# Kernel tuning notes

Hardware: AMD Instinct MI355X
Metric: run time of the kernel (lower is better)

## Reference

```python
import jax, jax.numpy as jnp
import numpy as np
from jax import lax


def setup_inputs() -> dict:
    key = jax.random.key(0)
    ks = jax.random.split(key, 8)
    B, N, q = 16, 4096, 256
    sc = float(1.0 / np.sqrt(q))
    return {
        "u": jax.random.normal(ks[0], (B, N, q), jnp.float32),
        "a": jax.random.normal(ks[1], (q,), jnp.float32),  # diag of A
        "W_B": jax.random.normal(ks[2], (q, q), jnp.float32) * sc,
        "b_B": jax.random.normal(ks[3], (q,), jnp.float32) * sc,
        "W_C": jax.random.normal(ks[4], (q, q), jnp.float32) * sc,
        "b_C": jax.random.normal(ks[5], (q,), jnp.float32) * sc,
        "W_D": jax.random.normal(ks[6], (q, q), jnp.float32) * sc,
        "b_D": jax.random.normal(ks[7], (q,), jnp.float32) * sc,
    }


def _solve_im(u, a, W_B, b_B, dt):
    """IM solver. A is diagonal, so M_inv is four diagonal blocks:
    new_x = s*x - dt*s*a*z ; new_z = dt*s*x + s*z, with s = 1/(1+dt^2*a).
    Forcing F = M_inv @ [dt*B(u); 0] -> (dt*s*Bu, dt^2*s*Bu)."""
    s = 1.0 / (1.0 + dt * dt * a)  # (q,)
    Bu = jnp.einsum("bnq,pq->bnp", u, W_B) + b_B  # (B,N,q), torch Linear: u @ W^T + b
    f_x = (dt * s) * Bu
    f_z = (dt * dt * s) * Bu
    dsa = dt * s * a
    ds = dt * s

    def step(carry, f):
        x, z = carry
        fx, fz = f
        x_new = s * x - dsa * z + fx
        z_new = ds * x + s * z + fz
        return (x_new, z_new), z_new

    Bsz, _, q = u.shape
    init = (jnp.zeros((Bsz, q), u.dtype), jnp.zeros((Bsz, q), u.dtype))
    # scan over time axis
    _, z_t = lax.scan(step, init, (jnp.moveaxis(f_x, 1, 0), jnp.moveaxis(f_z, 1, 0)))
    return jnp.moveaxis(z_t, 0, 1)  # (B,N,q) -- the out[..., size:] half


def reference(u, a, W_B, b_B, W_C, b_C, W_D, b_D):
    N = u.shape[1]
    dt = 1.0 / N
    y = _solve_im(u, a, W_B, b_B, dt)
    x = (jnp.einsum("bnq,pq->bnp", y, W_C) + b_C) + (jnp.einsum("bnq,pq->bnp", u, W_D) + b_D)
    x = jax.nn.gelu(x, approximate=False)  # torch GELU default = exact erf
    # GLU(concat([x, x], -1)) == x * sigmoid(x)
    out = x * jax.nn.sigmoid(x) + u
    return (out, y)
```

## Files before the change

kernel.cpp:

```cpp
#include <hip/hip_runtime.h>
#include <hip/hip_bf16.h>
#include <cstdint>

typedef __bf16 bf16_t;
typedef __bf16 bf16x8 __attribute__((ext_vector_type(8)));
typedef float f32x4 __attribute__((ext_vector_type(4)));

#define B_SZ 16
#define N_SZ 4096
#define Q_SZ 256
#define M_TOT (B_SZ * N_SZ)
#define DT (1.0f / 4096.0f)
#define LDST 40
#define CHUNKS 16
#define CLEN (N_SZ / CHUNKS)

__device__ __forceinline__ bf16x8 load8f(const float* p) {
  const float4 v0 = *(const float4*)p;
  const float4 v1 = *(const float4*)(p + 4);
  bf16x8 v;
  v[0] = (bf16_t)v0.x; v[1] = (bf16_t)v0.y; v[2] = (bf16_t)v0.z; v[3] = (bf16_t)v0.w;
  v[4] = (bf16_t)v1.x; v[5] = (bf16_t)v1.y; v[6] = (bf16_t)v1.z; v[7] = (bf16_t)v1.w;
  return v;
}

__device__ __forceinline__ void kloop(const float* __restrict__ Ap,
                                      const float* __restrict__ Bp,
                                      int m0, int n0, int t,
                                      bf16_t* As, bf16_t* Bs, f32x4 acc[4][4]) {
  const int r = t >> 2, cc = t & 3;
  const int lane = t & 63, ln = lane & 15, quad = lane >> 4;
  const int wave = t >> 6;
  const int wm = (wave & 1) * 64, wn = (wave >> 1) * 64;

  for (int k0 = 0; k0 < Q_SZ; k0 += 32) {
#pragma unroll
    for (int i = 0; i < 2; ++i) {
      const int row = r + i * 64;
      const int col = k0 + cc * 8;
      *(bf16x8*)(As + row * LDST + cc * 8) =
          load8f(Ap + (size_t)(m0 + row) * Q_SZ + col);
      *(bf16x8*)(Bs + row * LDST + cc * 8) =
          load8f(Bp + (size_t)(n0 + row) * Q_SZ + col);
    }
    __syncthreads();
    bf16x8 af[4], bv[4];
#pragma unroll
    for (int mi = 0; mi < 4; ++mi) {
      af[mi] = *(const bf16x8*)(As + (wm + mi * 16 + ln) * LDST + quad * 8);
      bv[mi] = *(const bf16x8*)(Bs + (wn + mi * 16 + ln) * LDST + quad * 8);
    }
#pragma unroll
    for (int mi = 0; mi < 4; ++mi)
#pragma unroll
      for (int ni = 0; ni < 4; ++ni)
        acc[mi][ni] = __builtin_amdgcn_mfma_f32_16x16x32_bf16(af[mi], bv[ni],
                                                              acc[mi][ni], 0, 0, 0);
    __syncthreads();
  }
}

__global__ __launch_bounds__(256) void gemm1_kernel(
    const float* __restrict__ u, const float* __restrict__ WB,
    const float* __restrict__ a, const float* __restrict__ bB,
    float* __restrict__ fx) {
  __shared__ __align__(16) bf16_t As[128 * LDST];
  __shared__ __align__(16) bf16_t Bs[128 * LDST];
  const int t = threadIdx.x;
  const int m0 = blockIdx.x * 128, n0 = blockIdx.y * 128;
  f32x4 acc[4][4] = {};
  kloop(u, WB, m0, n0, t, As, Bs, acc);

  const int lane = t & 63, ln = lane & 15, quad = lane >> 4;
  const int wave = t >> 6;
  const int wm = (wave & 1) * 64, wn = (wave >> 1) * 64;
#pragma unroll
  for (int ni = 0; ni < 4; ++ni) {
    const int gp = n0 + wn + ni * 16 + ln;
    const float av = a[gp];
    const float s = 1.0f / (1.0f + DT * DT * av);
    const float sc = DT * s;
    const float bb = bB[gp];
#pragma unroll
    for (int mi = 0; mi < 4; ++mi) {
      const int gm = m0 + wm + mi * 16 + quad * 4;
#pragma unroll
      for (int r2 = 0; r2 < 4; ++r2)
        fx[(size_t)(gm + r2) * Q_SZ + gp] = sc * (acc[mi][ni][r2] + bb);
    }
  }
}

#define PF 8

__global__ __launch_bounds__(256) void scan1_kernel(
    const float* __restrict__ fx, const float* __restrict__ a,
    float* __restrict__ ex, float* __restrict__ ez) {
  const int g = blockIdx.x * 256 + threadIdx.x;
  const int p = g & 255, c = (g >> 8) & (CHUNKS - 1), b = g >> 12;
  const float av = a[p];
  const float s = 1.0f / (1.0f + DT * DT * av);
  const float dsa = DT * s * av, dss = DT * s;
  float x = 0.f, z = 0.f;
  const float* fp = fx + ((size_t)b * N_SZ + c * CLEN) * Q_SZ + p;
  float buf[PF], nbuf[PF];
#pragma unroll
  for (int j = 0; j < PF; ++j) buf[j] = fp[(size_t)j * Q_SZ];
  for (int n = 0; n < CLEN; n += PF) {
    if (n + PF < CLEN) {
#pragma unroll
      for (int j = 0; j < PF; ++j) nbuf[j] = fp[(size_t)(n + PF + j) * Q_SZ];
    }
#pragma unroll
    for (int j = 0; j < PF; ++j) {
      const float f = buf[j];
      const float xn = fmaf(s, x, fmaf(-dsa, z, f));
      const float zn = fmaf(dss, x, fmaf(s, z, DT * f));
      x = xn; z = zn;
    }
#pragma unroll
    for (int j = 0; j < PF; ++j) buf[j] = nbuf[j];
  }
  ex[g] = x; ez[g] = z;
}

__global__ __launch_bounds__(256) void scan2_kernel(
    const float* __restrict__ a, const float* __restrict__ ex,
    const float* __restrict__ ez, float* __restrict__ ix, float* __restrict__ iz) {
  const int g = blockIdx.x * 256 + threadIdx.x;
  const int p = g & 255, b = g >> 8;
  const float av = a[p];
  const float s = 1.0f / (1.0f + DT * DT * av);
  float m00 = s, m01 = -DT * s * av, m10 = DT * s, m11 = s;
#pragma unroll
  for (int i = 0; i < 8; ++i) {
    const float a00 = fmaf(m00, m00, m01 * m10);
    const float a01 = m01 * (m00 + m11);
    const float a10 = m10 * (m00 + m11);
    const float a11 = fmaf(m11, m11, m01 * m10);
    m00 = a00; m01 = a01; m10 = a10; m11 = a11;
  }
  float x = 0.f, z = 0.f;
  for (int c = 0; c < CHUNKS; ++c) {
    const size_t idx = ((size_t)b * CHUNKS + c) * Q_SZ + p;
    ix[idx] = x; iz[idx] = z;
    const float xn = fmaf(m00, x, fmaf(m01, z, ex[idx]));
    const float zn = fmaf(m10, x, fmaf(m11, z, ez[idx]));
    x = xn; z = zn;
  }
}

__global__ __launch_bounds__(256) void scan3_kernel(
    const float* __restrict__ a, const float* __restrict__ ix,
    const float* __restrict__ iz, float* __restrict__ yf) {
  const int g = blockIdx.x * 256 + threadIdx.x;
  const int p = g & 255, c = (g >> 8) & (CHUNKS - 1), b = g >> 12;
  const float av = a[p];
  const float s = 1.0f / (1.0f + DT * DT * av);
  const float dsa = DT * s * av, dss = DT * s;
  float x = ix[g], z = iz[g];
  float* yp = yf + ((size_t)b * N_SZ + c * CLEN) * Q_SZ + p;
  float buf[PF], nbuf[PF];
#pragma unroll
  for (int j = 0; j < PF; ++j) buf[j] = yp[(size_t)j * Q_SZ];
  for (int n = 0; n < CLEN; n += PF) {
    if (n + PF < CLEN) {
#pragma unroll
      for (int j = 0; j < PF; ++j) nbuf[j] = yp[(size_t)(n + PF + j) * Q_SZ];
    }
#pragma unroll
    for (int j = 0; j < PF; ++j) {
      const float f = buf[j];
      const float xn = fmaf(s, x, fmaf(-dsa, z, f));
      const float zn = fmaf(dss, x, fmaf(s, z, DT * f));
      x = xn; z = zn;
      yp[(size_t)(n + j) * Q_SZ] = zn;
    }
#pragma unroll
    for (int j = 0; j < PF; ++j) buf[j] = nbuf[j];
  }
}

__global__ __launch_bounds__(256) void scan_mono_kernel(
    const float* __restrict__ a, float* __restrict__ yf) {
  const int g = blockIdx.x * 256 + threadIdx.x;
  const int p = g & 255, b = g >> 8;
  const float av = a[p];
  const float s = 1.0f / (1.0f + DT * DT * av);
  const float dsa = DT * s * av, dss = DT * s;
  float x = 0.f, z = 0.f;
  float* yp = yf + (size_t)b * N_SZ * Q_SZ + p;
  float buf[PF], nbuf[PF];
#pragma unroll
  for (int j = 0; j < PF; ++j) buf[j] = yp[(size_t)j * Q_SZ];
  for (int n = 0; n < N_SZ; n += PF) {
    if (n + PF < N_SZ) {
#pragma unroll
      for (int j = 0; j < PF; ++j) nbuf[j] = yp[(size_t)(n + PF + j) * Q_SZ];
    }
#pragma unroll
    for (int j = 0; j < PF; ++j) {
      const float f = buf[j];
      const float xn = fmaf(s, x, fmaf(-dsa, z, f));
      const float zn = fmaf(dss, x, fmaf(s, z, DT * f));
      x = xn; z = zn;
      yp[(size_t)(n + j) * Q_SZ] = zn;
    }
#pragma unroll
    for (int j = 0; j < PF; ++j) buf[j] = nbuf[j];
  }
}

__global__ __launch_bounds__(256) void gemm2_kernel(
    const float* __restrict__ y, const float* __restrict__ WC,
    const float* __restrict__ u, const float* __restrict__ WD,
    const float* __restrict__ bC, const float* __restrict__ bD,
    float* __restrict__ out0) {
  __shared__ __align__(16) bf16_t As[128 * LDST];
  __shared__ __align__(16) bf16_t Bs[128 * LDST];
  const int t = threadIdx.x;
  const int m0 = blockIdx.x * 128, n0 = blockIdx.y * 128;
  f32x4 acc[4][4] = {};
  kloop(y, WC, m0, n0, t, As, Bs, acc);
  kloop(u, WD, m0, n0, t, As, Bs, acc);

  const int lane = t & 63, ln = lane & 15, quad = lane >> 4;
  const int wave = t >> 6;
  const int wm = (wave & 1) * 64, wn = (wave >> 1) * 64;
#pragma unroll
  for (int ni = 0; ni < 4; ++ni) {
    const int gp = n0 + wn + ni * 16 + ln;
    const float bias = bC[gp] + bD[gp];
#pragma unroll
    for (int mi = 0; mi < 4; ++mi) {
      const int gm = m0 + wm + mi * 16 + quad * 4;
#pragma unroll
      for (int r2 = 0; r2 < 4; ++r2) {
        const float x = acc[mi][ni][r2] + bias;
        const float g = 0.5f * x * (1.0f + erff(x * 0.70710678118654752f));
        const float sg = 1.0f / (1.0f + __expf(-g));
        const float uu = u[(size_t)(gm + r2) * Q_SZ + gp];
        out0[(size_t)(gm + r2) * Q_SZ + gp] = fmaf(g, sg, uu);
      }
    }
  }
}

extern "C" void kernel_launch(void* const* d_in, const int* in_sizes, int n_in,
                              void* d_out, int out_size, void* d_ws, size_t ws_size,
                              hipStream_t stream) {
  const float* u  = (const float*)d_in[0];
  const float* a  = (const float*)d_in[1];
  const float* WB = (const float*)d_in[2];
  const float* bB = (const float*)d_in[3];
  const float* WC = (const float*)d_in[4];
  const float* bC = (const float*)d_in[5];
  const float* WD = (const float*)d_in[6];
  const float* bD = (const float*)d_in[7];

  float* out0 = (float*)d_out;
  float* yreg = out0 + (size_t)M_TOT * Q_SZ;

  dim3 gg(M_TOT / 128, Q_SZ / 128);
  gemm1_kernel<<<gg, 256, 0, stream>>>(u, WB, a, bB, yreg);

  const size_t state_bytes = 4 * (size_t)M_TOT * sizeof(float);
  if (ws_size >= state_bytes) {
    float* ex = (float*)d_ws;
    float* ez = ex + M_TOT;
    float* ix = ez + M_TOT;
    float* iz = ix + M_TOT;
    scan1_kernel<<<256, 256, 0, stream>>>(yreg, a, ex, ez);
    scan2_kernel<<<16, 256, 0, stream>>>(a, ex, ez, ix, iz);
    scan3_kernel<<<256, 256, 0, stream>>>(a, ix, iz, yreg);
  } else {
    scan_mono_kernel<<<16, 256, 0, stream>>>(a, yreg);
  }

  gemm2_kernel<<<gg, 256, 0, stream>>>(yreg, WC, u, WD, bC, bD, out0);
}
```

Measured before the change: 329.7 us.

## Pre-convert operands to bf16 and use double-buffered direct-to-LDS GEMM loads

Adds a prep kernel that converts u and the three weight matrices to bf16 in workspace, and has scan3 also write a bf16 copy of y. The GEMMs then stage tiles with global_load_lds into XOR-swizzled, double-buffered LDS and use a swizzled block order. The aim is to halve GEMM operand traffic, overlap loads with MFMA work, and remove per-tile float-to-bf16 conversion. In exchange it adds an extra pass over u, extra bf16 writes in the scan, and a much larger workspace requirement, falling back to the old path when the workspace is too small.

```diff
diff --git a/kernel.cpp b/kernel.cpp
--- a/kernel.cpp
+++ b/kernel.cpp
@@ -14,6 +14,8 @@
 #define LDST 40
 #define CHUNKS 16
 #define CLEN (N_SZ / CHUNKS)
+#define PF 8
+
 
 __device__ __forceinline__ bf16x8 load8f(const float* p) {
   const float4 v0 = *(const float4*)p;
@@ -24,53 +26,93 @@
   return v;
 }
 
-__device__ __forceinline__ void kloop(const float* __restrict__ Ap,
-                                      const float* __restrict__ Bp,
-                                      int m0, int n0, int t,
-                                      bf16_t* As, bf16_t* Bs, f32x4 acc[4][4]) {
-  const int r = t >> 2, cc = t & 3;
-  const int lane = t & 63, ln = lane & 15, quad = lane >> 4;
-  const int wave = t >> 6;
-  const int wm = (wave & 1) * 64, wn = (wave >> 1) * 64;
-
-  for (int k0 = 0; k0 < Q_SZ; k0 += 32) {
-#pragma unroll
-    for (int i = 0; i < 2; ++i) {
-      const int row = r + i * 64;
-      const int col = k0 + cc * 8;
-      *(bf16x8*)(As + row * LDST + cc * 8) =
-          load8f(Ap + (size_t)(m0 + row) * Q_SZ + col);
-      *(bf16x8*)(Bs + row * LDST + cc * 8) =
-          load8f(Bp + (size_t)(n0 + row) * Q_SZ + col);
-    }
-    __syncthreads();
-    bf16x8 af[4], bv[4];
-#pragma unroll
-    for (int mi = 0; mi < 4; ++mi) {
-      af[mi] = *(const bf16x8*)(As + (wm + mi * 16 + ln) * LDST + quad * 8);
-      bv[mi] = *(const bf16x8*)(Bs + (wn + mi * 16 + ln) * LDST + quad * 8);
-    }
-#pragma unroll
-    for (int mi = 0; mi < 4; ++mi)
-#pragma unroll
-      for (int ni = 0; ni < 4; ++ni)
-        acc[mi][ni] = __builtin_amdgcn_mfma_f32_16x16x32_bf16(af[mi], bv[ni],
-                                                              acc[mi][ni], 0, 0, 0);
-    __syncthreads();
-  }
-}
-
-__global__ __launch_bounds__(256) void gemm1_kernel(
+__device__ __forceinline__ void gll16(const bf16_t* g, bf16_t* l) {
+  __builtin_amdgcn_global_load_lds(
+      (const __attribute__((address_space(1))) void*)g,
+      (__attribute__((address_space(3))) void*)l, 16, 0, 0);
+}
+
+
+__device__ __forceinline__ void stage2(const bf16_t* __restrict__ A,
+                                       const bf16_t* __restrict__ Bm,
+                                       int m0, int n0, int k0, int t,
+                                       bf16_t* As, bf16_t* Bs) {
+#pragma unroll
+  for (int j = 0; j < 2; ++j) {
+    const int i = j * 256 + t;
+    const int row = i >> 2;
+    const int cpos = i & 3;
+    const int cdat = cpos ^ ((row >> 1) & 3);
+    bf16_t* la = As + (size_t)i * 8;
+    bf16_t* lb = Bs + (size_t)i * 8;
+    gll16(A + (size_t)(m0 + row) * Q_SZ + k0 + cdat * 8, la);
+    gll16(Bm + (size_t)(n0 + row) * Q_SZ + k0 + cdat * 8, lb);
+  }
+}
+
+__device__ __forceinline__ void mstep(const bf16_t* As, const bf16_t* Bs,
+                                      int t, f32x4 acc[4][4]) {
+  const int lane = t & 63, ln = lane & 15, quad = lane >> 4;
+  const int wave = t >> 6;
+  const int wm = (wave & 1) * 64, wn = (wave >> 1) * 64;
+  const int csw = (quad ^ ((ln >> 1) & 3)) * 8;
+  bf16x8 af[4], bv[4];
+#pragma unroll
+  for (int mi = 0; mi < 4; ++mi) {
+    af[mi] = *(const bf16x8*)(As + (wm + mi * 16 + ln) * 32 + csw);
+    bv[mi] = *(const bf16x8*)(Bs + (wn + mi * 16 + ln) * 32 + csw);
+  }
+#pragma unroll
+  for (int mi = 0; mi < 4; ++mi)
+#pragma unroll
+    for (int ni = 0; ni < 4; ++ni)
+      acc[mi][ni] = __builtin_amdgcn_mfma_f32_16x16x32_bf16(af[mi], bv[ni],
+                                                            acc[mi][ni], 0, 0, 0);
+}
+
+__global__ __launch_bounds__(256) void prep_kernel(
     const float* __restrict__ u, const float* __restrict__ WB,
+    const float* __restrict__ WC, const float* __restrict__ WD,
+    bf16_t* __restrict__ ub, bf16_t* __restrict__ WBb,
+    bf16_t* __restrict__ WCb, bf16_t* __restrict__ WDb) {
+  const int g = blockIdx.x * 256 + threadIdx.x;
+  const int UC = (M_TOT * Q_SZ) / 8;
+  const float* src;
+  bf16_t* dst;
+  int idx;
+  if (g < UC) {
+    src = u; dst = ub; idx = g;
+  } else {
+    const int h = g - UC;
+    const int w = h >> 13;
+    idx = h & 8191;
+    src = (w == 0) ? WB : (w == 1) ? WC : WD;
+    dst = (w == 0) ? WBb : (w == 1) ? WCb : WDb;
+  }
+  *(bf16x8*)(dst + (size_t)idx * 8) = load8f(src + (size_t)idx * 8);
+}
+
+__global__ __launch_bounds__(256) void gemm1b_kernel(
+    const bf16_t* __restrict__ ub, const bf16_t* __restrict__ WBb,
     const float* __restrict__ a, const float* __restrict__ bB,
     float* __restrict__ fx) {
-  __shared__ __align__(16) bf16_t As[128 * LDST];
-  __shared__ __align__(16) bf16_t Bs[128 * LDST];
+  __shared__ __align__(16) bf16_t As[2][128 * 32];
+  __shared__ __align__(16) bf16_t Bs[2][128 * 32];
   const int t = threadIdx.x;
-  const int m0 = blockIdx.x * 128, n0 = blockIdx.y * 128;
+  const int bid = blockIdx.x;
+  const int swz = (bid & 7) * 128 + (bid >> 3);
+  const int m0 = (swz >> 1) * 128, n0 = (swz & 1) * 128;
   f32x4 acc[4][4] = {};
-  kloop(u, WB, m0, n0, t, As, Bs, acc);
-
+  stage2(ub, WBb, m0, n0, 0, t, As[0], Bs[0]);
+  __syncthreads();
+#pragma unroll 2
+  for (int k = 0; k < 8; ++k) {
+    const int cur = k & 1;
+    if (k < 7)
+      stage2(ub, WBb, m0, n0, (k + 1) * 32, t, As[cur ^ 1], Bs[cur ^ 1]);
+    mstep(As[cur], Bs[cur], t, acc);
+    __syncthreads();
+  }
   const int lane = t & 63, ln = lane & 15, quad = lane >> 4;
   const int wave = t >> 6;
   const int wm = (wave & 1) * 64, wn = (wave >> 1) * 64;
@@ -91,7 +133,54 @@
   }
 }
 
-#define PF 8
+__global__ __launch_bounds__(256) void gemm2b_kernel(
+    const bf16_t* __restrict__ yb, const bf16_t* __restrict__ WCb,
+    const bf16_t* __restrict__ ub, const bf16_t* __restrict__ WDb,
+    const float* __restrict__ u, const float* __restrict__ bC,
+    const float* __restrict__ bD, float* __restrict__ out0) {
+  __shared__ __align__(16) bf16_t As[2][128 * 32];
+  __shared__ __align__(16) bf16_t Bs[2][128 * 32];
+  const int t = threadIdx.x;
+  const int bid = blockIdx.x;
+  const int swz = (bid & 7) * 128 + (bid >> 3);
+  const int m0 = (swz >> 1) * 128, n0 = (swz & 1) * 128;
+  f32x4 acc[4][4] = {};
+  stage2(yb, WCb, m0, n0, 0, t, As[0], Bs[0]);
+  __syncthreads();
+#pragma unroll 2
+  for (int kk = 0; kk < 16; ++kk) {
+    const int cur = kk & 1;
+    if (kk < 15) {
+      const int nk = kk + 1;
+      const bf16_t* Ap = (nk < 8) ? yb : ub;
+      const bf16_t* Bp = (nk < 8) ? WCb : WDb;
+      stage2(Ap, Bp, m0, n0, (nk & 7) * 32, t, As[cur ^ 1], Bs[cur ^ 1]);
+    }
+    mstep(As[cur], Bs[cur], t, acc);
+    __syncthreads();
+  }
+  const int lane = t & 63, ln = lane & 15, quad = lane >> 4;
+  const int wave = t >> 6;
+  const int wm = (wave & 1) * 64, wn = (wave >> 1) * 64;
+#pragma unroll
+  for (int ni = 0; ni < 4; ++ni) {
+    const int gp = n0 + wn + ni * 16 + ln;
+    const float bias = bC[gp] + bD[gp];
+#pragma unroll
+    for (int mi = 0; mi < 4; ++mi) {
+      const int gm = m0 + wm + mi * 16 + quad * 4;
+#pragma unroll
+      for (int r2 = 0; r2 < 4; ++r2) {
+        const float x = acc[mi][ni][r2] + bias;
+        const float g = 0.5f * x * (1.0f + erff(x * 0.70710678118654752f));
+        const float sg = 1.0f / (1.0f + __expf(-g));
+        const float uu = u[(size_t)(gm + r2) * Q_SZ + gp];
+        out0[(size_t)(gm + r2) * Q_SZ + gp] = fmaf(g, sg, uu);
+      }
+    }
+  }
+}
+
 
 __global__ __launch_bounds__(256) void scan1_kernel(
     const float* __restrict__ fx, const float* __restrict__ a,
@@ -152,14 +241,17 @@
 
 __global__ __launch_bounds__(256) void scan3_kernel(
     const float* __restrict__ a, const float* __restrict__ ix,
-    const float* __restrict__ iz, float* __restrict__ yf) {
+    const float* __restrict__ iz, float* __restrict__ yf,
+    bf16_t* __restrict__ yb) {
   const int g = blockIdx.x * 256 + threadIdx.x;
   const int p = g & 255, c = (g >> 8) & (CHUNKS - 1), b = g >> 12;
   const float av = a[p];
   const float s = 1.0f / (1.0f + DT * DT * av);
   const float dsa = DT * s * av, dss = DT * s;
   float x = ix[g], z = iz[g];
-  float* yp = yf + ((size_t)b * N_SZ + c * CLEN) * Q_SZ + p;
+  const size_t base = ((size_t)b * N_SZ + c * CLEN) * Q_SZ + p;
+  float* yp = yf + base;
+  bf16_t* ybp = yb ? yb + base : nullptr;
   float buf[PF], nbuf[PF];
 #pragma unroll
   for (int j = 0; j < PF; ++j) buf[j] = yp[(size_t)j * Q_SZ];
@@ -175,6 +267,7 @@
       const float zn = fmaf(dss, x, fmaf(s, z, DT * f));
       x = xn; z = zn;
       yp[(size_t)(n + j) * Q_SZ] = zn;
+      if (yb) ybp[(size_t)(n + j) * Q_SZ] = (bf16_t)zn;
     }
 #pragma unroll
     for (int j = 0; j < PF; ++j) buf[j] = nbuf[j];
@@ -208,6 +301,74 @@
     }
 #pragma unroll
     for (int j = 0; j < PF; ++j) buf[j] = nbuf[j];
+  }
+}
+
+
+__device__ __forceinline__ void kloop(const float* __restrict__ Ap,
+                                      const float* __restrict__ Bp,
+                                      int m0, int n0, int t,
+                                      bf16_t* As, bf16_t* Bs, f32x4 acc[4][4]) {
+  const int r = t >> 2, cc = t & 3;
+  const int lane = t & 63, ln = lane & 15, quad = lane >> 4;
+  const int wave = t >> 6;
+  const int wm = (wave & 1) * 64, wn = (wave >> 1) * 64;
+
+  for (int k0 = 0; k0 < Q_SZ; k0 += 32) {
+#pragma unroll
+    for (int i = 0; i < 2; ++i) {
+      const int row = r + i * 64;
+      const int col = k0 + cc * 8;
+      *(bf16x8*)(As + row * LDST + cc * 8) =
+          load8f(Ap + (size_t)(m0 + row) * Q_SZ + col);
+      *(bf16x8*)(Bs + row * LDST + cc * 8) =
+          load8f(Bp + (size_t)(n0 + row) * Q_SZ + col);
+    }
+    __syncthreads();
+    bf16x8 af[4], bv[4];
+#pragma unroll
+    for (int mi = 0; mi < 4; ++mi) {
+      af[mi] = *(const bf16x8*)(As + (wm + mi * 16 + ln) * LDST + quad * 8);
+      bv[mi] = *(const bf16x8*)(Bs + (wn + mi * 16 + ln) * LDST + quad * 8);
+    }
+#pragma unroll
+    for (int mi = 0; mi < 4; ++mi)
+#pragma unroll
+      for (int ni = 0; ni < 4; ++ni)
+        acc[mi][ni] = __builtin_amdgcn_mfma_f32_16x16x32_bf16(af[mi], bv[ni],
+                                                              acc[mi][ni], 0, 0, 0);
+    __syncthreads();
+  }
+}
+
+__global__ __launch_bounds__(256) void gemm1_kernel(
+    const float* __restrict__ u, const float* __restrict__ WB,
+    const float* __restrict__ a, const float* __restrict__ bB,
+    float* __restrict__ fx) {
+  __shared__ __align__(16) bf16_t As[128 * LDST];
+  __shared__ __align__(16) bf16_t Bs[128 * LDST];
+  const int t = threadIdx.x;
+  const int m0 = blockIdx.x * 128, n0 = blockIdx.y * 128;
+  f32x4 acc[4][4] = {};
+  kloop(u, WB, m0, n0, t, As, Bs, acc);
+
+  const int lane = t & 63, ln = lane & 15, quad = lane >> 4;
+  const int wave = t >> 6;
+  const int wm = (wave & 1) * 64, wn = (wave >> 1) * 64;
+#pragma unroll
+  for (int ni = 0; ni < 4; ++ni) {
+    const int gp = n0 + wn + ni * 16 + ln;
+    const float av = a[gp];
+    const float s = 1.0f / (1.0f + DT * DT * av);
+    const float sc = DT * s;
+    const float bb = bB[gp];
+#pragma unroll
+    for (int mi = 0; mi < 4; ++mi) {
+      const int gm = m0 + wm + mi * 16 + quad * 4;
+#pragma unroll
+      for (int r2 = 0; r2 < 4; ++r2)
+        fx[(size_t)(gm + r2) * Q_SZ + gp] = sc * (acc[mi][ni][r2] + bb);
+    }
   }
 }
 
@@ -246,6 +407,7 @@
   }
 }
 
+
 extern "C" void kernel_launch(void* const* d_in, const int* in_sizes, int n_in,
                               void* d_out, int out_size, void* d_ws, size_t ws_size,
                               hipStream_t stream) {
@@ -261,21 +423,43 @@
   float* out0 = (float*)d_out;
   float* yreg = out0 + (size_t)M_TOT * Q_SZ;
 
-  dim3 gg(M_TOT / 128, Q_SZ / 128);
-  gemm1_kernel<<<gg, 256, 0, stream>>>(u, WB, a, bB, yreg);
-
+  const size_t UB_ELEMS = (size_t)M_TOT * Q_SZ;
+  const size_t W_ELEMS = (size_t)Q_SZ * Q_SZ;
   const size_t state_bytes = 4 * (size_t)M_TOT * sizeof(float);
-  if (ws_size >= state_bytes) {
-    float* ex = (float*)d_ws;
+  const size_t need_full =
+      (2 * UB_ELEMS + 3 * W_ELEMS) * sizeof(bf16_t) + state_bytes;
+
+  if (ws_size >= need_full) {
+    bf16_t* ub  = (bf16_t*)d_ws;
+    bf16_t* yb  = ub + UB_ELEMS;
+    bf16_t* WBb = yb + UB_ELEMS;
+    bf16_t* WCb = WBb + W_ELEMS;
+    bf16_t* WDb = WCb + W_ELEMS;
+    float* ex = (float*)(WDb + W_ELEMS);
     float* ez = ex + M_TOT;
     float* ix = ez + M_TOT;
     float* iz = ix + M_TOT;
+
+    prep_kernel<<<8288, 256, 0, stream>>>(u, WB, WC, WD, ub, WBb, WCb, WDb);
+    gemm1b_kernel<<<1024, 256, 0, stream>>>(ub, WBb, a, bB, yreg);
     scan1_kernel<<<256, 256, 0, stream>>>(yreg, a, ex, ez);
     scan2_kernel<<<16, 256, 0, stream>>>(a, ex, ez, ix, iz);
-    scan3_kernel<<<256, 256, 0, stream>>>(a, ix, iz, yreg);
+    scan3_kernel<<<256, 256, 0, stream>>>(a, ix, iz, yreg, yb);
+    gemm2b_kernel<<<1024, 256, 0, stream>>>(yb, WCb, ub, WDb, u, bC, bD, out0);
   } else {
-    scan_mono_kernel<<<16, 256, 0, stream>>>(a, yreg);
-  }
-
-  gemm2_kernel<<<gg, 256, 0, stream>>>(yreg, WC, u, WD, bC, bD, out0);
-}
+    dim3 gg(M_TOT / 128, Q_SZ / 128);
+    gemm1_kernel<<<gg, 256, 0, stream>>>(u, WB, a, bB, yreg);
+    if (ws_size >= state_bytes) {
+      float* ex = (float*)d_ws;
+      float* ez = ex + M_TOT;
+      float* ix = ez + M_TOT;
+      float* iz = ix + M_TOT;
+      scan1_kernel<<<256, 256, 0, stream>>>(yreg, a, ex, ez);
+      scan2_kernel<<<16, 256, 0, stream>>>(a, ex, ez, ix, iz);
+      scan3_kernel<<<256, 256, 0, stream>>>(a, ix, iz, yreg, (bf16_t*)nullptr);
+    } else {
+      scan_mono_kernel<<<16, 256, 0, stream>>>(a, yreg);
+    }
+    gemm2_kernel<<<gg, 256, 0, stream>>>(yreg, WC, u, WD, bC, bD, out0);
+  }
+}
```

Result: slower. 357.4 us (+8.4%).
